# Kernel tuning notes

Hardware: AMD Instinct MI355X
Metric: run time of the kernel (lower is better)

The kernel has to match this reference:

```python
import math
import jax, jax.numpy as jnp
import numpy as np

D_MODEL = 768
N_HEADS = 12
HEAD_DIM = D_MODEL // N_HEADS
D_FF = 3072
LN_EPS = 1e-5


def _alibi_slopes(n_heads):
    def pow2(n):
        start = 2 ** (-(2 ** (-(math.log2(n) - 3))))
        return [start * start ** i for i in range(n)]
    if n_heads & (n_heads - 1) == 0:
        s = pow2(n_heads)
    else:
        c = 2 ** math.floor(math.log2(n_heads))
        s = pow2(c) + pow2(2 * c)[0::2][: n_heads - c]
    return np.asarray(s, dtype=np.float32)  # positive; negated at use site


def _ln(t, g, b):
    m = jnp.mean(t, axis=-1, keepdims=True)
    v = jnp.mean(jnp.square(t - m), axis=-1, keepdims=True)
    return (t - m) * jax.lax.rsqrt(v + LN_EPS) * g + b


def setup_inputs() -> dict:
    key = jax.random.key(0)
    ks = jax.random.split(key, 12)
    B, N = 4, 1025
    s = 0.02
    inp = {
        "x": jax.random.normal(ks[0], (B, N, D_MODEL), dtype=jnp.float32),
        "positions": jax.random.normal(ks[1], (B, N, 2), dtype=jnp.float32) * 8.0,
        "patch_sizes": jax.random.uniform(ks[2], (B,), dtype=jnp.float32, minval=0.5, maxval=2.0),
        "num_registers": 0,
        "ln1_g": jnp.ones((D_MODEL,), jnp.float32),
        "ln1_b": jnp.zeros((D_MODEL,), jnp.float32),
        "wq": jax.random.normal(ks[3], (D_MODEL, D_MODEL), jnp.float32) * s,
        "bq": jnp.zeros((D_MODEL,), jnp.float32),
        "wk": jax.random.normal(ks[4], (D_MODEL, D_MODEL), jnp.float32) * s,
        "bk": jnp.zeros((D_MODEL,), jnp.float32),
        "wv": jax.random.normal(ks[5], (D_MODEL, D_MODEL), jnp.float32) * s,
        "bv": jnp.zeros((D_MODEL,), jnp.float32),
        "wo": jax.random.normal(ks[6], (D_MODEL, D_MODEL), jnp.float32) * s,
        "bo": jnp.zeros((D_MODEL,), jnp.float32),
        "qn_g": jnp.ones((HEAD_DIM,), jnp.float32),
        "qn_b": jnp.zeros((HEAD_DIM,), jnp.float32),
        "kn_g": jnp.ones((HEAD_DIM,), jnp.float32),
        "kn_b": jnp.zeros((HEAD_DIM,), jnp.float32),
        "ln2_g": jnp.ones((D_MODEL,), jnp.float32),
        "ln2_b": jnp.zeros((D_MODEL,), jnp.float32),
        "w1": jax.random.normal(ks[7], (D_MODEL, D_FF), jnp.float32) * s,
        "b1": jnp.zeros((D_FF,), jnp.float32),
        "w2": jax.random.normal(ks[8], (D_FF, D_MODEL), jnp.float32) * s,
        "b2": jnp.zeros((D_MODEL,), jnp.float32),
    }
    return inp


def reference(x, positions, patch_sizes, num_registers,
              ln1_g, ln1_b, wq, bq, wk, bk, wv, bv, wo, bo,
              qn_g, qn_b, kn_g, kn_b, ln2_g, ln2_b, w1, b1, w2, b2):
    B, N, d = x.shape
    H, HD = N_HEADS, HEAD_DIM

    xn = _ln(x, ln1_g, ln1_b)
    q = (xn @ wq + bq).reshape(B, N, H, HD).transpose(0, 2, 1, 3)  # [B,H,N,HD]
    k = (xn @ wk + bk).reshape(B, N, H, HD).transpose(0, 2, 1, 3)
    v = (xn @ wv + bv).reshape(B, N, H, HD).transpose(0, 2, 1, 3)
    q = _ln(q, qn_g, qn_b)  # qk-norm over head_dim
    k = _ln(k, kn_g, kn_b)

    # 2-D ALiBi bias: [B,H,N,N]
    slopes = jnp.asarray(_alibi_slopes(H))  # positive
    ps = jnp.clip(patch_sizes, 1e-6)[:, None, None]
    diff = positions[:, :, None, :] - positions[:, None, :, :]  # [B,N,N,2]
    dist = jnp.sqrt(jnp.sum(jnp.square(diff), axis=-1)) / ps  # [B,N,N]
    bias = -slopes[None, :, None, None] * dist[:, None, :, :]
    idx = jnp.arange(N)
    special = (idx == 0) | ((idx >= 1) & (idx < 1 + num_registers))  # CLS + registers
    keep = (~special).astype(x.dtype)
    bias = bias * keep[None, None, :, None] * keep[None, None, None, :]

    scale = 1.0 / math.sqrt(HD)
    scores = jnp.einsum('bhqd,bhkd->bhqk', q, k) * scale + bias
    attn = jax.nn.softmax(scores, axis=-1)
    o = jnp.einsum('bhqk,bhkd->bhqd', attn, v)
    o = o.transpose(0, 2, 1, 3).reshape(B, N, d) @ wo + bo
    x = x + o

    xn2 = _ln(x, ln2_g, ln2_b)
    mlp = jax.nn.gelu(xn2 @ w1 + b1, approximate=False) @ w2 + b2
    return x + mlp
```

## Files before the change

### kernel.cpp

```cpp
#include <hip/hip_runtime.h>
#include <hip/hip_bf16.h>
#include <math.h>

typedef __attribute__((ext_vector_type(4))) float f32x4;
typedef __attribute__((ext_vector_type(8))) short short8;

#define DMODEL 768
#define NH 12
#define HD 64
#define DFF 3072
#define KVB 64
#define NSPLIT 3
#define QH 2
#define NP 1040

struct FalseC { static constexpr bool v = false; };
struct TrueC  { static constexpr bool v = true;  };

__device__ __forceinline__ short f2bf(float f) {
    union { float f; unsigned int u; } c; c.f = f;
    unsigned int r = c.u + 0x7FFFu + ((c.u >> 16) & 1u);
    return (short)(r >> 16);
}

__device__ __forceinline__ float bf2f(short s) {
    union { unsigned int u; float f; } c; c.u = ((unsigned int)(unsigned short)s) << 16;
    return c.f;
}

__device__ __forceinline__ void gload16(const void* g, void* l) {
    __builtin_amdgcn_global_load_lds((const __attribute__((address_space(1))) void*)g,
                                     (__attribute__((address_space(3))) void*)l, 16, 0, 0);
}

__device__ __forceinline__ int xcd_swz(int o, int nwg) {
    int q = nwg >> 3, r = nwg & 7, x = o & 7, i = o >> 3;
    return (x < r ? x * (q + 1) : r * (q + 1) + (x - r) * q) + i;
}

__global__ __launch_bounds__(256) void transpose_cast(const float* __restrict__ src,
                                                      short* __restrict__ dst, int K, int Nn) {
    __shared__ float tile[32][33];
    const int n0 = blockIdx.x * 32, k0 = blockIdx.y * 32;
    const int tx = threadIdx.x & 31, ty = threadIdx.x >> 5;
    #pragma unroll
    for (int i = ty; i < 32; i += 8) {
        int k = k0 + i, n = n0 + tx;
        tile[i][tx] = (k < K && n < Nn) ? src[(size_t)k * Nn + n] : 0.f;
    }
    __syncthreads();
    #pragma unroll
    for (int i = ty; i < 32; i += 8) {
        int n = n0 + i, k = k0 + tx;
        if (n < Nn && k < K) dst[(size_t)n * K + k] = f2bf(tile[tx][i]);
    }
}

__global__ void concat_bias(const float* __restrict__ bq, const float* __restrict__ bk,
                            const float* __restrict__ bv, float* __restrict__ out) {
    int i = blockIdx.x * 256 + threadIdx.x;
    if (i < 2304) out[i] = (i < 768) ? bq[i] : (i < 1536 ? bk[i - 768] : bv[i - 1536]);
}

__global__ __launch_bounds__(256) void ln_rows(const float* __restrict__ x, const float* __restrict__ g,
                                               const float* __restrict__ bb, short* __restrict__ out, int M) {
    __shared__ float red[8];
    const int row = blockIdx.x;
    const int tid = threadIdx.x;
    const float* xr = x + (size_t)row * DMODEL;
    float v[3];
    #pragma unroll
    for (int j = 0; j < 3; j++) v[j] = xr[tid + j * 256];
    float s = v[0] + v[1] + v[2];
    #pragma unroll
    for (int mk = 32; mk; mk >>= 1) s += __shfl_xor(s, mk);
    if ((tid & 63) == 0) red[tid >> 6] = s;
    __syncthreads();
    const float mean = (red[0] + red[1] + red[2] + red[3]) * (1.0f / 768.0f);
    float sq = 0.f;
    #pragma unroll
    for (int j = 0; j < 3; j++) { float d = v[j] - mean; sq += d * d; }
    #pragma unroll
    for (int mk = 32; mk; mk >>= 1) sq += __shfl_xor(sq, mk);
    if ((tid & 63) == 0) red[4 + (tid >> 6)] = sq;
    __syncthreads();
    const float var = (red[4] + red[5] + red[6] + red[7]) * (1.0f / 768.0f);
    const float rstd = rsqrtf(var + 1e-5f);
    short* orow = out + (size_t)row * DMODEL;
    #pragma unroll
    for (int j = 0; j < 3; j++) {
        int col = tid + j * 256;
        orow[col] = f2bf((v[j] - mean) * rstd * g[col] + bb[col]);
    }
}

__global__ __launch_bounds__(256) void gemm_qkv(const short* __restrict__ A, const short* __restrict__ Bt,
        const float* __restrict__ bias,
        const float* __restrict__ qg, const float* __restrict__ qb2,
        const float* __restrict__ kg, const float* __restrict__ kb2,
        short* __restrict__ Qb, short* __restrict__ Kb, short* __restrict__ Vtp,
        int M, int B, int Nseq) {
    __shared__ short As[64 * 64];
    __shared__ short Bs[128 * 64];
    const int nbx = 18, nby = (M + 63) / 64;
    const int sid = xcd_swz(blockIdx.x, nbx * nby);
    const int n0 = (sid % nbx) * 128, m0 = (sid / nbx) * 64;
    const int tid = threadIdx.x, w = tid >> 6, lane = tid & 63, g = lane >> 4, cl = lane & 15;
    const int wm = w >> 1, wn = w & 1;
    f32x4 acc[2][4];
    #pragma unroll
    for (int a = 0; a < 2; a++)
        #pragma unroll
        for (int b2 = 0; b2 < 4; b2++) acc[a][b2] = (f32x4){0.f, 0.f, 0.f, 0.f};
    for (int kk = 0; kk < 768; kk += 64) {
        #pragma unroll
        for (int c = 0; c < 1536; c += 256) {
            int ci = c + tid;
            if (ci < 512) {
                int row = ci >> 3, p = ci & 7;
                int arow = m0 + row; if (arow >= M) arow = M - 1;
                gload16(A + (size_t)arow * 768 + kk + ((p ^ (row & 7)) << 3), &As[ci * 8]);
            } else {
                int c2 = ci - 512;
                int row = c2 >> 3, p = c2 & 7;
                gload16(Bt + (size_t)(n0 + row) * 768 + kk + ((p ^ (row & 7)) << 3), &Bs[c2 * 8]);
            }
        }
        __syncthreads();
        #pragma unroll
        for (int kh = 0; kh < 2; ++kh) {
            short8 af[2], bf[4];
            #pragma unroll
            for (int mi = 0; mi < 2; mi++) {
                int ra = wm * 32 + mi * 16 + cl;
                af[mi] = *(const short8*)&As[ra * 64 + ((((kh << 2) + g) ^ (ra & 7)) << 3)];
            }
            #pragma unroll
            for (int ni = 0; ni < 4; ni++) {
                int rb = wn * 64 + ni * 16 + cl;
                bf[ni] = *(const short8*)&Bs[rb * 64 + ((((kh << 2) + g) ^ (rb & 7)) << 3)];
            }
            #pragma unroll
            for (int mi = 0; mi < 2; mi++)
                #pragma unroll
                for (int ni = 0; ni < 4; ni++)
                    acc[mi][ni] = __builtin_amdgcn_mfma_f32_16x16x32_bf16(af[mi], bf[ni], acc[mi][ni], 0, 0, 0);
        }
        __syncthreads();
    }
    const int t = n0 / 768;
    const int h = (n0 - t * 768) / 64 + wn;
    const int b0 = m0 / Nseq, bnd = (b0 + 1) * Nseq;
    float bi[4];
    #pragma unroll
    for (int ni = 0; ni < 4; ni++) bi[ni] = bias[n0 + wn * 64 + ni * 16 + cl];
    if (t < 2) {
        const float* gp = (t == 0) ? qg : kg;
        const float* bp = (t == 0) ? qb2 : kb2;
        float gv[4], bv[4];
        #pragma unroll
        for (int ni = 0; ni < 4; ni++) { gv[ni] = gp[ni * 16 + cl]; bv[ni] = bp[ni * 16 + cl]; }
        short* out = (t == 0) ? Qb : Kb;
        #pragma unroll
        for (int mi = 0; mi < 2; mi++)
            #pragma unroll
            for (int r = 0; r < 4; r++) {
                int row = m0 + wm * 32 + mi * 16 + 4 * g + r;
                float v0 = acc[mi][0][r] + bi[0];
                float v1 = acc[mi][1][r] + bi[1];
                float v2 = acc[mi][2][r] + bi[2];
                float v3 = acc[mi][3][r] + bi[3];
                float sx = v0 + v1 + v2 + v3;
                float sxx = v0 * v0 + v1 * v1 + v2 * v2 + v3 * v3;
                #pragma unroll
                for (int mk = 8; mk; mk >>= 1) { sx += __shfl_xor(sx, mk); sxx += __shfl_xor(sxx, mk); }
                float mean = sx * (1.0f / 64.0f);
                float var = sxx * (1.0f / 64.0f) - mean * mean;
                float rstd = rsqrtf(var + 1e-5f);
                if (row < M) {
                    int bb = (row >= bnd) ? b0 + 1 : b0;
                    int n = row - bb * Nseq;
                    size_t base = (((size_t)bb * NH + h) * Nseq + n) * HD + cl;
                    out[base + 0]  = f2bf(fmaf((v0 - mean) * rstd, gv[0], bv[0]));
                    out[base + 16] = f2bf(fmaf((v1 - mean) * rstd, gv[1], bv[1]));
                    out[base + 32] = f2bf(fmaf((v2 - mean) * rstd, gv[2], bv[2]));
                    out[base + 48] = f2bf(fmaf((v3 - mean) * rstd, gv[3], bv[3]));
                }
            }
    } else {
        #pragma unroll
        for (int mi = 0; mi < 2; mi++)
            #pragma unroll
            for (int r = 0; r < 4; r++) {
                int row = m0 + wm * 32 + mi * 16 + 4 * g + r;
                if (row < M) {
                    int bb = (row >= bnd) ? b0 + 1 : b0;
                    int n = row - bb * Nseq;
                    size_t vb2 = ((size_t)bb * NH + h) * HD + cl;
                    #pragma unroll
                    for (int ni = 0; ni < 4; ni++)
                        Vtp[(vb2 + ni * 16) * NP + n] = f2bf(acc[mi][ni][r] + bi[ni]);
                }
            }
    }
}

template<int EPI, int BM, int BN>
__global__ __launch_bounds__(256) void gemm_bt(const short* __restrict__ A, const short* __restrict__ Bt,
        const float* __restrict__ bias, const float* __restrict__ res, void* __restrict__ Cv,
        int M, int Nn, int K) {
    constexpr int RN = BN / 32;
    __shared__ short As[BM * 64];
    __shared__ short Bs[BN * 64];
    const int nbx = Nn / BN, nby = (M + BM - 1) / BM;
    const int sid = xcd_swz(blockIdx.x, nbx * nby);
    const int n0 = (sid % nbx) * BN, m0 = (sid / nbx) * BM;
    const int tid = threadIdx.x, w = tid >> 6, lane = tid & 63, g = lane >> 4, cl = lane & 15;
    const int wm = w >> 1, wn = w & 1;
    f32x4 acc[2][RN];
    #pragma unroll
    for (int a = 0; a < 2; a++)
        #pragma unroll
        for (int b2 = 0; b2 < RN; b2++) acc[a][b2] = (f32x4){0.f, 0.f, 0.f, 0.f};
    constexpr int CHA = BM * 8, CHT = (BM + BN) * 8;
    for (int kk = 0; kk < K; kk += 64) {
        #pragma unroll
        for (int c = 0; c < CHT; c += 256) {
            int ci = c + tid;
            if (ci < CHA) {
                int row = ci >> 3, p = ci & 7;
                int arow = m0 + row; if (arow >= M) arow = M - 1;
                gload16(A + (size_t)arow * K + kk + ((p ^ (row & 7)) << 3), &As[ci * 8]);
            } else {
                int c2 = ci - CHA;
                int row = c2 >> 3, p = c2 & 7;
                gload16(Bt + (size_t)(n0 + row) * K + kk + ((p ^ (row & 7)) << 3), &Bs[c2 * 8]);
            }
        }
        __syncthreads();
        #pragma unroll
        for (int kh = 0; kh < 2; ++kh) {
            short8 af[2], bf[RN];
            #pragma unroll
            for (int mi = 0; mi < 2; mi++) {
                int ra = wm * (BM / 2) + mi * 16 + cl;
                af[mi] = *(const short8*)&As[ra * 64 + ((((kh << 2) + g) ^ (ra & 7)) << 3)];
            }
            #pragma unroll
            for (int ni = 0; ni < RN; ni++) {
                int rb = wn * (BN / 2) + ni * 16 + cl;
                bf[ni] = *(const short8*)&Bs[rb * 64 + ((((kh << 2) + g) ^ (rb & 7)) << 3)];
            }
            #pragma unroll
            for (int mi = 0; mi < 2; mi++)
                #pragma unroll
                for (int ni = 0; ni < RN; ni++)
                    acc[mi][ni] = __builtin_amdgcn_mfma_f32_16x16x32_bf16(af[mi], bf[ni], acc[mi][ni], 0, 0, 0);
        }
        __syncthreads();
    }
    #pragma unroll
    for (int ni = 0; ni < RN; ++ni) {
        int col = n0 + wn * (BN / 2) + ni * 16 + cl;
        float bi = bias[col];
        #pragma unroll
        for (int mi = 0; mi < 2; ++mi) {
            int rb = m0 + wm * (BM / 2) + mi * 16 + 4 * g;
            #pragma unroll
            for (int r = 0; r < 4; ++r) {
                int row = rb + r;
                if (row < M) {
                    float vv = acc[mi][ni][r] + bi;
                    if (EPI == 1) {
                        vv += res[(size_t)row * Nn + col];
                        ((float*)Cv)[(size_t)row * Nn + col] = vv;
                    } else {
                        float ge = 0.5f * vv * (1.0f + erff(vv * 0.70710678118654752f));
                        ((short*)Cv)[(size_t)row * Nn + col] = f2bf(ge);
                    }
                }
            }
        }
    }
}

__global__ __launch_bounds__(256, 3) void attn_kernel(
        const short* __restrict__ Qb, const short* __restrict__ Kb, const short* __restrict__ Vt,
        const float* __restrict__ pos, const float* __restrict__ psz, const int* __restrict__ nregp,
        short* __restrict__ opart, float* __restrict__ ppart, int B, int Nn, int nwg) {
    __shared__ short Vbuf[2][QH][4096];
    __shared__ short Pl[4][QH][16][72];
    __shared__ float Rs[4][QH][16];
    const int nqt = (Nn + 63) >> 6;
    const int sid = xcd_swz(blockIdx.x, nwg);
    const int qt = sid % nqt;
    const int rem = sid / nqt;
    const int nyy = (NH / QH) * NSPLIT;
    const int yy = rem % nyy;
    const int b = rem / nyy;
    const int h0 = (yy / NSPLIT) * QH, sp = yy % NSPLIT;
    const int tid = threadIdx.x, w = tid >> 6, lane = tid & 63, g = lane >> 4, cl = lane & 15;
    const int nreg1 = 1 + nregp[0];
    const float inv_ps = 1.0f / fmaxf(psz[b], 1e-6f);
    const float sc2 = 0.125f * 1.4426950408889634f;
    const size_t bq = (size_t)b * Nn;
    const float2* __restrict__ pos2 = (const float2*)pos;
    const int q0 = qt * 64 + w * 16;

    size_t bh[QH], vb[QH];
    short8 qa[QH][2];
    float sP[QH];
    int qr = q0 + cl; if (qr > Nn - 1) qr = Nn - 1;
    const float2 qp = pos2[bq + qr];
    const float keepq = (qr < nreg1) ? 0.f : 1.f;
    #pragma unroll
    for (int hh = 0; hh < QH; hh++) {
        int h = h0 + hh;
        bh[hh] = ((size_t)b * NH + h) * (size_t)Nn;
        vb[hh] = ((size_t)b * NH + h) * (size_t)(HD * NP);
        float slope = (h < 8) ? exp2f(-(float)(h + 1)) : exp2f(-0.5f - (float)(h - 8));
        sP[hh] = slope * inv_ps * 1.4426950408889634f * keepq;
        const short* qptr = Qb + (bh[hh] + qr) * HD;
        qa[hh][0] = *(const short8*)(qptr + 8 * g);
        qa[hh][1] = *(const short8*)(qptr + 32 + 8 * g);
    }

    int qi[4];
    #pragma unroll
    for (int i = 0; i < 4; i++) qi[i] = q0 + 4 * g + i;

    f32x4 o[QH][4];
    float psum[QH] = {0.f, 0.f};
    #pragma unroll
    for (int hh = 0; hh < QH; hh++)
        #pragma unroll
        for (int c2 = 0; c2 < 4; c2++) o[hh][c2] = (f32x4){0.f, 0.f, 0.f, 0.f};

    const int ktiles = (Nn + KVB - 1) / KVB;
    const int tps = (ktiles + NSPLIT - 1) / NSPLIT;
    const int t0 = sp * tps, t1 = min(ktiles, t0 + tps);

    auto stage = [&](int buf, int kt) {
        const int kv0 = kt * KVB;
        #pragma unroll
        for (int it = 0; it < 2 * QH; ++it) {
            int idx = it * 256 + tid;
            int hh = idx >> 9, rm = idx & 511;
            int d = rm >> 3, slot = rm & 7;
            int kvs = kv0 + ((slot ^ (d & 7)) << 3);
            gload16(Vt + vb[hh] + (size_t)d * NP + kvs, &Vbuf[buf][hh][rm * 8]);
        }
    };

    stage(0, t0);
    int cur = 0;
    for (int kt = t0; kt < t1; ++kt) {
        const int kv0 = kt * KVB;
        __syncthreads();
        if (kt + 1 < t1) stage(cur ^ 1, kt + 1);

        auto qbody = [&](int qt2, auto mc, auto tc) {
            constexpr bool KMASK = decltype(mc)::v;
            constexpr bool TAIL  = decltype(tc)::v;
            const int kbase = kv0 + qt2 * 16;
            int krow = kbase + cl;
            if (TAIL) krow = min(krow, Nn - 1);
            const short* kp0 = Kb + (bh[0] + krow) * HD;
            const short* kp1 = Kb + (bh[1] + krow) * HD;
            const short8 k00 = *(const short8*)(kp0 + 8 * g);
            const short8 k01 = *(const short8*)(kp0 + 32 + 8 * g);
            const short8 k10 = *(const short8*)(kp1 + 8 * g);
            const short8 k11 = *(const short8*)(kp1 + 32 + 8 * g);
            f32x4 s0 = __builtin_amdgcn_mfma_f32_16x16x32_bf16(k00, qa[0][0], (f32x4){0.f,0.f,0.f,0.f}, 0, 0, 0);
            s0 = __builtin_amdgcn_mfma_f32_16x16x32_bf16(k01, qa[0][1], s0, 0, 0, 0);
            f32x4 s1 = __builtin_amdgcn_mfma_f32_16x16x32_bf16(k10, qa[1][0], (f32x4){0.f,0.f,0.f,0.f}, 0, 0, 0);
            s1 = __builtin_amdgcn_mfma_f32_16x16x32_bf16(k11, qa[1][1], s1, 0, 0, 0);
            const int kb4 = kbase + 4 * g;
            float p0v[4], p1v[4];
            #pragma unroll
            for (int i = 0; i < 4; i++) {
                int ki = kb4 + i;
                int kic = TAIL ? min(ki, Nn - 1) : ki;
                float2 kp2 = pos2[bq + kic];
                float dx = qp.x - kp2.x, dy = qp.y - kp2.y;
                float dist = sqrtf(fmaf(dx, dx, dy * dy));
                if (KMASK) dist *= (ki < nreg1) ? 0.f : 1.f;
                float e0 = fmaf(s0[i], sc2, -12.0f);
                e0 = fmaf(-sP[0], dist, e0);
                float p0 = exp2f(e0);
                float e1 = fmaf(s1[i], sc2, -12.0f);
                e1 = fmaf(-sP[1], dist, e1);
                float p1 = exp2f(e1);
                if (TAIL) { bool vl = ki < Nn; p0 = vl ? p0 : 0.f; p1 = vl ? p1 : 0.f; }
                psum[0] += p0; psum[1] += p1;
                p0v[i] = p0; p1v[i] = p1;
            }
            unsigned int w00, w01, w10, w11;
            asm("v_cvt_pk_bf16_f32 %0, %1, %2" : "=v"(w00) : "v"(p0v[0]), "v"(p0v[1]));
            asm("v_cvt_pk_bf16_f32 %0, %1, %2" : "=v"(w01) : "v"(p0v[2]), "v"(p0v[3]));
            asm("v_cvt_pk_bf16_f32 %0, %1, %2" : "=v"(w10) : "v"(p1v[0]), "v"(p1v[1]));
            asm("v_cvt_pk_bf16_f32 %0, %1, %2" : "=v"(w11) : "v"(p1v[2]), "v"(p1v[3]));
            *(unsigned int*)&Pl[w][0][cl][qt2 * 16 + 4 * g]     = w00;
            *(unsigned int*)&Pl[w][0][cl][qt2 * 16 + 4 * g + 2] = w01;
            *(unsigned int*)&Pl[w][1][cl][qt2 * 16 + 4 * g]     = w10;
            *(unsigned int*)&Pl[w][1][cl][qt2 * 16 + 4 * g + 2] = w11;
        };

        const bool istail = (kv0 + KVB > Nn);
        if (!istail) {
            if (kv0 < nreg1) {
                qbody(0, TrueC{}, FalseC{}); qbody(1, TrueC{}, FalseC{});
                qbody(2, TrueC{}, FalseC{}); qbody(3, TrueC{}, FalseC{});
            } else {
                qbody(0, FalseC{}, FalseC{}); qbody(1, FalseC{}, FalseC{});
                qbody(2, FalseC{}, FalseC{}); qbody(3, FalseC{}, FalseC{});
            }
        } else {
            qbody(0, FalseC{}, TrueC{}); qbody(1, FalseC{}, TrueC{});
            qbody(2, FalseC{}, TrueC{}); qbody(3, FalseC{}, TrueC{});
        }

        #pragma unroll
        for (int hh = 0; hh < QH; hh++) {
            #pragma unroll
            for (int ks = 0; ks < 2; ++ks) {
                const short8 pf = *(const short8*)&Pl[w][hh][cl][ks * 32 + 8 * g];
                #pragma unroll
                for (int c2 = 0; c2 < 4; c2++) {
                    const int d = c2 * 16 + cl;
                    const int slot = ((ks << 2) + g) ^ (cl & 7);
                    const short8 vf = *(const short8*)&Vbuf[cur][hh][d * 64 + slot * 8];
                    o[hh][c2] = __builtin_amdgcn_mfma_f32_16x16x32_bf16(pf, vf, o[hh][c2], 0, 0, 0);
                }
            }
        }
        cur ^= 1;
    }

    #pragma unroll
    for (int hh = 0; hh < QH; hh++) {
        float r = psum[hh];
        r += __shfl_xor(r, 16);
        r += __shfl_xor(r, 32);
        if (lane < 16) Rs[w][hh][lane] = r;
    }
    float4 rs0 = *(const float4*)&Rs[w][0][4 * g];
    float4 rs1 = *(const float4*)&Rs[w][1][4 * g];
    #pragma unroll
    for (int i = 0; i < 4; i++) {
        if (qi[i] < Nn) {
            #pragma unroll
            for (int hh = 0; hh < QH; hh++) {
                size_t rbase = (((size_t)sp * B + b) * NH + (h0 + hh)) * Nn + qi[i];
                #pragma unroll
                for (int c2 = 0; c2 < 4; c2++)
                    opart[rbase * HD + c2 * 16 + cl] = f2bf(o[hh][c2][i]);
                if (cl == 0) ppart[rbase] = hh ? rs1[i] : rs0[i];
            }
        }
    }
}

__global__ __launch_bounds__(256) void attn_reduce(const short* __restrict__ opart,
        const float* __restrict__ ppart, short* __restrict__ Ob, int B, int Nn) {
    const int rows = B * NH * Nn;
    const int row = blockIdx.x * 4 + (threadIdx.x >> 6);
    if (row >= rows) return;
    const int d = threadIdx.x & 63;
    const int n = row % Nn;
    const int bh = row / Nn;
    const int h = bh % NH, b = bh / NH;
    const size_t stride = (size_t)B * NH * Nn;
    float o = 0.f, p = 0.f;
    #pragma unroll
    for (int s = 0; s < NSPLIT; s++) {
        o += bf2f(opart[((size_t)s * stride + row) * HD + d]);
        p += ppart[(size_t)s * stride + row];
    }
    Ob[((size_t)b * Nn + n) * DMODEL + h * HD + d] = f2bf(o / p);
}

extern "C" void kernel_launch(void* const* d_in, const int* in_sizes, int n_in,
                              void* d_out, int out_size, void* d_ws, size_t ws_size,
                              hipStream_t stream) {
    const float* x    = (const float*)d_in[0];
    const float* pos  = (const float*)d_in[1];
    const float* psz  = (const float*)d_in[2];
    const int*   nreg = (const int*)d_in[3];
    const float* ln1g = (const float*)d_in[4];
    const float* ln1b = (const float*)d_in[5];
    const float* wq   = (const float*)d_in[6];
    const float* bq   = (const float*)d_in[7];
    const float* wk   = (const float*)d_in[8];
    const float* bk   = (const float*)d_in[9];
    const float* wv   = (const float*)d_in[10];
    const float* bv   = (const float*)d_in[11];
    const float* wo   = (const float*)d_in[12];
    const float* bo   = (const float*)d_in[13];
    const float* qng  = (const float*)d_in[14];
    const float* qnb  = (const float*)d_in[15];
    const float* kng  = (const float*)d_in[16];
    const float* knb  = (const float*)d_in[17];
    const float* ln2g = (const float*)d_in[18];
    const float* ln2b = (const float*)d_in[19];
    const float* w1   = (const float*)d_in[20];
    const float* b1   = (const float*)d_in[21];
    const float* w2   = (const float*)d_in[22];
    const float* b2   = (const float*)d_in[23];

    const int B  = in_sizes[2];
    const int Nn = in_sizes[1] / (2 * B);
    const int M  = B * Nn;

    char* ws = (char*)d_ws;
    size_t off = 0;
    auto alloc = [&](size_t bytes) -> char* {
        char* p = ws + off;
        off += (bytes + 255) & ~(size_t)255;
        return p;
    };
    short* wt_qkv   = (short*)alloc((size_t)2304 * 768 * 2);
    short* wt_o     = (short*)alloc((size_t)768 * 768 * 2);
    short* wt_1     = (short*)alloc((size_t)3072 * 768 * 2);
    short* wt_2     = (short*)alloc((size_t)768 * 3072 * 2);
    float* bias_qkv = (float*)alloc(2304 * 4);
    short* xn       = (short*)alloc((size_t)M * 768 * 2);
    short* Qb       = (short*)alloc((size_t)M * 768 * 2);
    short* Kb       = (short*)alloc((size_t)M * 768 * 2);
    short* Vt       = (short*)alloc((size_t)B * NH * HD * NP * 2 + 4096);
    short* Ob       = (short*)alloc((size_t)M * 768 * 2);
    float* x1       = (float*)alloc((size_t)M * 768 * 4);
    short* xn2      = (short*)alloc((size_t)M * 768 * 2);
    short* hmid     = (short*)alloc((size_t)M * 3072 * 2);
    float* ppart    = (float*)alloc((size_t)NSPLIT * B * NH * Nn * 4);
    short* opart    = hmid;

    dim3 blk(256);
    transpose_cast<<<dim3(24, 24), blk, 0, stream>>>(wq, wt_qkv, 768, 768);
    transpose_cast<<<dim3(24, 24), blk, 0, stream>>>(wk, wt_qkv + 768 * 768, 768, 768);
    transpose_cast<<<dim3(24, 24), blk, 0, stream>>>(wv, wt_qkv + 2 * 768 * 768, 768, 768);
    transpose_cast<<<dim3(24, 24), blk, 0, stream>>>(wo, wt_o, 768, 768);
    transpose_cast<<<dim3(96, 24), blk, 0, stream>>>(w1, wt_1, 768, 3072);
    transpose_cast<<<dim3(24, 96), blk, 0, stream>>>(w2, wt_2, 3072, 768);
    concat_bias<<<9, blk, 0, stream>>>(bq, bk, bv, bias_qkv);

    const int MB64 = (M + 63) / 64;
    ln_rows<<<M, blk, 0, stream>>>(x, ln1g, ln1b, xn, M);
    gemm_qkv<<<18 * MB64, blk, 0, stream>>>(xn, wt_qkv, bias_qkv, qng, qnb, kng, knb,
                                            Qb, Kb, Vt, M, B, Nn);
    const int nqt = (Nn + 63) / 64;
    const int anwg = nqt * (NH / QH) * NSPLIT * B;
    attn_kernel<<<anwg, blk, 0, stream>>>(Qb, Kb, Vt, pos, psz, nreg, opart, ppart, B, Nn, anwg);
    attn_reduce<<<(B * NH * Nn + 3) / 4, blk, 0, stream>>>(opart, ppart, Ob, B, Nn);
    gemm_bt<1, 64, 64><<<12 * MB64, blk, 0, stream>>>(Ob, wt_o, bo, x, x1, M, 768, 768);
    ln_rows<<<M, blk, 0, stream>>>(x1, ln2g, ln2b, xn2, M);
    gemm_bt<2, 64, 128><<<24 * MB64, blk, 0, stream>>>(xn2, wt_1, b1, nullptr, hmid, M, 3072, 768);
    gemm_bt<1, 64, 64><<<12 * MB64, blk, 0, stream>>>(hmid, wt_2, b2, x1, (float*)d_out, M, 768, 3072);
}
```

Baseline: 264.7 us.

## Shrink attention KV tile to 32, pack both heads' V in one LDS buffer

The attention kernel now processes 32 keys per tile instead of 64, with 2 KV splits instead of 3. Both heads' V slices share one 64x64 swizzled LDS buffer, and the P scratch padding is reduced. Less shared memory and fewer registers let the launch bound rise to 4 blocks per CU, aimed at better latency hiding, at the cost of more loop iterations and barriers per key. The GEMM template is also generalized to support BM other than 64 via an RM parameter.

```diff
diff --git a/kernel.cpp b/kernel.cpp
--- a/kernel.cpp
+++ b/kernel.cpp
@@ -9,8 +9,8 @@
 #define NH 12
 #define HD 64
 #define DFF 3072
-#define KVB 64
-#define NSPLIT 3
+#define KVB 32
+#define NSPLIT 2
 #define QH 2
 #define NP 1040
 
@@ -209,7 +209,7 @@
 __global__ __launch_bounds__(256) void gemm_bt(const short* __restrict__ A, const short* __restrict__ Bt,
         const float* __restrict__ bias, const float* __restrict__ res, void* __restrict__ Cv,
         int M, int Nn, int K) {
-    constexpr int RN = BN / 32;
+    constexpr int RM = BM / 32, RN = BN / 32;
     __shared__ short As[BM * 64];
     __shared__ short Bs[BN * 64];
     const int nbx = Nn / BN, nby = (M + BM - 1) / BM;
@@ -217,9 +217,9 @@
     const int n0 = (sid % nbx) * BN, m0 = (sid / nbx) * BM;
     const int tid = threadIdx.x, w = tid >> 6, lane = tid & 63, g = lane >> 4, cl = lane & 15;
     const int wm = w >> 1, wn = w & 1;
-    f32x4 acc[2][RN];
-    #pragma unroll
-    for (int a = 0; a < 2; a++)
+    f32x4 acc[RM][RN];
+    #pragma unroll
+    for (int a = 0; a < RM; a++)
         #pragma unroll
         for (int b2 = 0; b2 < RN; b2++) acc[a][b2] = (f32x4){0.f, 0.f, 0.f, 0.f};
     constexpr int CHA = BM * 8, CHT = (BM + BN) * 8;
@@ -240,9 +240,9 @@
         __syncthreads();
         #pragma unroll
         for (int kh = 0; kh < 2; ++kh) {
-            short8 af[2], bf[RN];
-            #pragma unroll
-            for (int mi = 0; mi < 2; mi++) {
+            short8 af[RM], bf[RN];
+            #pragma unroll
+            for (int mi = 0; mi < RM; mi++) {
                 int ra = wm * (BM / 2) + mi * 16 + cl;
                 af[mi] = *(const short8*)&As[ra * 64 + ((((kh << 2) + g) ^ (ra & 7)) << 3)];
             }
@@ -252,7 +252,7 @@
                 bf[ni] = *(const short8*)&Bs[rb * 64 + ((((kh << 2) + g) ^ (rb & 7)) << 3)];
             }
             #pragma unroll
-            for (int mi = 0; mi < 2; mi++)
+            for (int mi = 0; mi < RM; mi++)
                 #pragma unroll
                 for (int ni = 0; ni < RN; ni++)
                     acc[mi][ni] = __builtin_amdgcn_mfma_f32_16x16x32_bf16(af[mi], bf[ni], acc[mi][ni], 0, 0, 0);
@@ -264,7 +264,7 @@
         int col = n0 + wn * (BN / 2) + ni * 16 + cl;
         float bi = bias[col];
         #pragma unroll
-        for (int mi = 0; mi < 2; ++mi) {
+        for (int mi = 0; mi < RM; ++mi) {
             int rb = m0 + wm * (BM / 2) + mi * 16 + 4 * g;
             #pragma unroll
             for (int r = 0; r < 4; ++r) {
@@ -284,12 +284,12 @@
     }
 }
 
-__global__ __launch_bounds__(256, 3) void attn_kernel(
+__global__ __launch_bounds__(256, 4) void attn_kernel(
         const short* __restrict__ Qb, const short* __restrict__ Kb, const short* __restrict__ Vt,
         const float* __restrict__ pos, const float* __restrict__ psz, const int* __restrict__ nregp,
         short* __restrict__ opart, float* __restrict__ ppart, int B, int Nn, int nwg) {
-    __shared__ short Vbuf[2][QH][4096];
-    __shared__ short Pl[4][QH][16][72];
+    __shared__ short Vbuf[2][4096];
+    __shared__ short Pl[4][QH][16][68];
     __shared__ float Rs[4][QH][16];
     const int nqt = (Nn + 63) >> 6;
     const int sid = xcd_swz(blockIdx.x, nwg);
@@ -343,12 +343,13 @@
     auto stage = [&](int buf, int kt) {
         const int kv0 = kt * KVB;
         #pragma unroll
-        for (int it = 0; it < 2 * QH; ++it) {
+        for (int it = 0; it < 2; ++it) {
             int idx = it * 256 + tid;
-            int hh = idx >> 9, rm = idx & 511;
-            int d = rm >> 3, slot = rm & 7;
-            int kvs = kv0 + ((slot ^ (d & 7)) << 3);
-            gload16(Vt + vb[hh] + (size_t)d * NP + kvs, &Vbuf[buf][hh][rm * 8]);
+            int d = idx >> 3, s = idx & 7;
+            int u = s ^ (d & 7);
+            int hh = u >> 2;
+            int kvs = kv0 + ((u & 3) << 3);
+            gload16(Vt + vb[hh] + (size_t)d * NP + kvs, &Vbuf[buf][idx * 8]);
         }
     };
 
@@ -408,30 +409,21 @@
 
         const bool istail = (kv0 + KVB > Nn);
         if (!istail) {
-            if (kv0 < nreg1) {
-                qbody(0, TrueC{}, FalseC{}); qbody(1, TrueC{}, FalseC{});
-                qbody(2, TrueC{}, FalseC{}); qbody(3, TrueC{}, FalseC{});
-            } else {
-                qbody(0, FalseC{}, FalseC{}); qbody(1, FalseC{}, FalseC{});
-                qbody(2, FalseC{}, FalseC{}); qbody(3, FalseC{}, FalseC{});
-            }
+            if (kv0 < nreg1) { qbody(0, TrueC{}, FalseC{});  qbody(1, TrueC{}, FalseC{}); }
+            else             { qbody(0, FalseC{}, FalseC{}); qbody(1, FalseC{}, FalseC{}); }
         } else {
             qbody(0, FalseC{}, TrueC{}); qbody(1, FalseC{}, TrueC{});
-            qbody(2, FalseC{}, TrueC{}); qbody(3, FalseC{}, TrueC{});
         }
 
         #pragma unroll
         for (int hh = 0; hh < QH; hh++) {
-            #pragma unroll
-            for (int ks = 0; ks < 2; ++ks) {
-                const short8 pf = *(const short8*)&Pl[w][hh][cl][ks * 32 + 8 * g];
-                #pragma unroll
-                for (int c2 = 0; c2 < 4; c2++) {
-                    const int d = c2 * 16 + cl;
-                    const int slot = ((ks << 2) + g) ^ (cl & 7);
-                    const short8 vf = *(const short8*)&Vbuf[cur][hh][d * 64 + slot * 8];
-                    o[hh][c2] = __builtin_amdgcn_mfma_f32_16x16x32_bf16(pf, vf, o[hh][c2], 0, 0, 0);
-                }
+            const short8 pf = *(const short8*)&Pl[w][hh][cl][8 * g];
+            #pragma unroll
+            for (int c2 = 0; c2 < 4; c2++) {
+                const int d = c2 * 16 + cl;
+                const int slot = (hh * 4 + g) ^ (cl & 7);
+                const short8 vf = *(const short8*)&Vbuf[cur][d * 64 + slot * 8];
+                o[hh][c2] = __builtin_amdgcn_mfma_f32_16x16x32_bf16(pf, vf, o[hh][c2], 0, 0, 0);
             }
         }
         cur ^= 1;
```

Measured after the change: 270.5 us. 2.2% more time.

## Double-buffer shared-memory tiles in GEMMs with prefetch of next K slice

Applied to the files above, without the earlier changes.

The QKV and generic GEMM kernels now use two shared-memory buffers. Each iteration issues the next K-slice load before computing on the current one, and one of the two barriers per iteration is dropped. The QKV GEMM and the FC1 GEMM shrink the K tile to 32 to keep shared memory in check, with a 4-way XOR swizzle. The attention P scratch row padding also changes from 72 to 68. The aim is to hide global-load latency behind MFMA work, at the cost of more loop iterations and possibly different LDS bank-conflict behaviour.

```diff
diff --git a/kernel.cpp b/kernel.cpp
--- a/kernel.cpp
+++ b/kernel.cpp
@@ -100,8 +100,8 @@
         const float* __restrict__ kg, const float* __restrict__ kb2,
         short* __restrict__ Qb, short* __restrict__ Kb, short* __restrict__ Vtp,
         int M, int B, int Nseq) {
-    __shared__ short As[64 * 64];
-    __shared__ short Bs[128 * 64];
+    __shared__ short As[2][64 * 32];
+    __shared__ short Bs[2][128 * 32];
     const int nbx = 18, nby = (M + 63) / 64;
     const int sid = xcd_swz(blockIdx.x, nbx * nby);
     const int n0 = (sid % nbx) * 128, m0 = (sid / nbx) * 64;
@@ -112,42 +112,47 @@
     for (int a = 0; a < 2; a++)
         #pragma unroll
         for (int b2 = 0; b2 < 4; b2++) acc[a][b2] = (f32x4){0.f, 0.f, 0.f, 0.f};
-    for (int kk = 0; kk < 768; kk += 64) {
-        #pragma unroll
-        for (int c = 0; c < 1536; c += 256) {
+
+    auto stage = [&](int buf, int kk) {
+        #pragma unroll
+        for (int c = 0; c < 768; c += 256) {
             int ci = c + tid;
-            if (ci < 512) {
-                int row = ci >> 3, p = ci & 7;
+            if (ci < 256) {
+                int row = ci >> 2, p = ci & 3;
                 int arow = m0 + row; if (arow >= M) arow = M - 1;
-                gload16(A + (size_t)arow * 768 + kk + ((p ^ (row & 7)) << 3), &As[ci * 8]);
+                gload16(A + (size_t)arow * 768 + kk + ((p ^ (row & 3)) << 3), &As[buf][ci * 8]);
             } else {
-                int c2 = ci - 512;
-                int row = c2 >> 3, p = c2 & 7;
-                gload16(Bt + (size_t)(n0 + row) * 768 + kk + ((p ^ (row & 7)) << 3), &Bs[c2 * 8]);
-            }
-        }
+                int c2 = ci - 256;
+                int row = c2 >> 2, p = c2 & 3;
+                gload16(Bt + (size_t)(n0 + row) * 768 + kk + ((p ^ (row & 3)) << 3), &Bs[buf][c2 * 8]);
+            }
+        }
+    };
+
+    stage(0, 0);
+    int cur = 0;
+    for (int kk = 0; kk < 768; kk += 32) {
         __syncthreads();
-        #pragma unroll
-        for (int kh = 0; kh < 2; ++kh) {
-            short8 af[2], bf[4];
-            #pragma unroll
-            for (int mi = 0; mi < 2; mi++) {
-                int ra = wm * 32 + mi * 16 + cl;
-                af[mi] = *(const short8*)&As[ra * 64 + ((((kh << 2) + g) ^ (ra & 7)) << 3)];
-            }
-            #pragma unroll
-            for (int ni = 0; ni < 4; ni++) {
-                int rb = wn * 64 + ni * 16 + cl;
-                bf[ni] = *(const short8*)&Bs[rb * 64 + ((((kh << 2) + g) ^ (rb & 7)) << 3)];
-            }
-            #pragma unroll
-            for (int mi = 0; mi < 2; mi++)
-                #pragma unroll
-                for (int ni = 0; ni < 4; ni++)
-                    acc[mi][ni] = __builtin_amdgcn_mfma_f32_16x16x32_bf16(af[mi], bf[ni], acc[mi][ni], 0, 0, 0);
-        }
-        __syncthreads();
-    }
+        if (kk + 32 < 768) stage(cur ^ 1, kk + 32);
+        short8 af[2], bf[4];
+        #pragma unroll
+        for (int mi = 0; mi < 2; mi++) {
+            int ra = wm * 32 + mi * 16 + cl;
+            af[mi] = *(const short8*)&As[cur][ra * 32 + ((g ^ (ra & 3)) << 3)];
+        }
+        #pragma unroll
+        for (int ni = 0; ni < 4; ni++) {
+            int rb = wn * 64 + ni * 16 + cl;
+            bf[ni] = *(const short8*)&Bs[cur][rb * 32 + ((g ^ (rb & 3)) << 3)];
+        }
+        #pragma unroll
+        for (int mi = 0; mi < 2; mi++)
+            #pragma unroll
+            for (int ni = 0; ni < 4; ni++)
+                acc[mi][ni] = __builtin_amdgcn_mfma_f32_16x16x32_bf16(af[mi], bf[ni], acc[mi][ni], 0, 0, 0);
+        cur ^= 1;
+    }
+
     const int t = n0 / 768;
     const int h = (n0 - t * 768) / 64 + wn;
     const int b0 = m0 / Nseq, bnd = (b0 + 1) * Nseq;
@@ -205,66 +210,74 @@
     }
 }
 
-template<int EPI, int BM, int BN>
+template<int EPI, int BM, int BN, int BK>
 __global__ __launch_bounds__(256) void gemm_bt(const short* __restrict__ A, const short* __restrict__ Bt,
         const float* __restrict__ bias, const float* __restrict__ res, void* __restrict__ Cv,
         int M, int Nn, int K) {
-    constexpr int RN = BN / 32;
-    __shared__ short As[BM * 64];
-    __shared__ short Bs[BN * 64];
+    constexpr int RM = BM / 32, RN = BN / 32;
+    constexpr int SL = BK / 8, SM = SL - 1;
+    __shared__ short As[2][BM * BK];
+    __shared__ short Bs[2][BN * BK];
     const int nbx = Nn / BN, nby = (M + BM - 1) / BM;
     const int sid = xcd_swz(blockIdx.x, nbx * nby);
     const int n0 = (sid % nbx) * BN, m0 = (sid / nbx) * BM;
     const int tid = threadIdx.x, w = tid >> 6, lane = tid & 63, g = lane >> 4, cl = lane & 15;
     const int wm = w >> 1, wn = w & 1;
-    f32x4 acc[2][RN];
-    #pragma unroll
-    for (int a = 0; a < 2; a++)
+    f32x4 acc[RM][RN];
+    #pragma unroll
+    for (int a = 0; a < RM; a++)
         #pragma unroll
         for (int b2 = 0; b2 < RN; b2++) acc[a][b2] = (f32x4){0.f, 0.f, 0.f, 0.f};
-    constexpr int CHA = BM * 8, CHT = (BM + BN) * 8;
-    for (int kk = 0; kk < K; kk += 64) {
+    constexpr int CHA = BM * SL, CHT = (BM + BN) * SL;
+
+    auto stage = [&](int buf, int kk) {
         #pragma unroll
         for (int c = 0; c < CHT; c += 256) {
             int ci = c + tid;
             if (ci < CHA) {
-                int row = ci >> 3, p = ci & 7;
+                int row = ci / SL, p = ci & SM;
                 int arow = m0 + row; if (arow >= M) arow = M - 1;
-                gload16(A + (size_t)arow * K + kk + ((p ^ (row & 7)) << 3), &As[ci * 8]);
+                gload16(A + (size_t)arow * K + kk + ((p ^ (row & SM)) << 3), &As[buf][ci * 8]);
             } else {
                 int c2 = ci - CHA;
-                int row = c2 >> 3, p = c2 & 7;
-                gload16(Bt + (size_t)(n0 + row) * K + kk + ((p ^ (row & 7)) << 3), &Bs[c2 * 8]);
-            }
-        }
+                int row = c2 / SL, p = c2 & SM;
+                gload16(Bt + (size_t)(n0 + row) * K + kk + ((p ^ (row & SM)) << 3), &Bs[buf][c2 * 8]);
+            }
+        }
+    };
+
+    stage(0, 0);
+    int cur = 0;
+    for (int kk = 0; kk < K; kk += BK) {
         __syncthreads();
-        #pragma unroll
-        for (int kh = 0; kh < 2; ++kh) {
-            short8 af[2], bf[RN];
-            #pragma unroll
-            for (int mi = 0; mi < 2; mi++) {
+        if (kk + BK < K) stage(cur ^ 1, kk + BK);
+        #pragma unroll
+        for (int kh = 0; kh < BK / 32; ++kh) {
+            short8 af[RM], bf[RN];
+            #pragma unroll
+            for (int mi = 0; mi < RM; mi++) {
                 int ra = wm * (BM / 2) + mi * 16 + cl;
-                af[mi] = *(const short8*)&As[ra * 64 + ((((kh << 2) + g) ^ (ra & 7)) << 3)];
+                af[mi] = *(const short8*)&As[cur][ra * BK + ((((kh << 2) + g) ^ (ra & SM)) << 3)];
             }
             #pragma unroll
             for (int ni = 0; ni < RN; ni++) {
                 int rb = wn * (BN / 2) + ni * 16 + cl;
-                bf[ni] = *(const short8*)&Bs[rb * 64 + ((((kh << 2) + g) ^ (rb & 7)) << 3)];
-            }
-            #pragma unroll
-            for (int mi = 0; mi < 2; mi++)
+                bf[ni] = *(const short8*)&Bs[cur][rb * BK + ((((kh << 2) + g) ^ (rb & SM)) << 3)];
+            }
+            #pragma unroll
+            for (int mi = 0; mi < RM; mi++)
                 #pragma unroll
                 for (int ni = 0; ni < RN; ni++)
                     acc[mi][ni] = __builtin_amdgcn_mfma_f32_16x16x32_bf16(af[mi], bf[ni], acc[mi][ni], 0, 0, 0);
         }
-        __syncthreads();
+        cur ^= 1;
     }
     #pragma unroll
     for (int ni = 0; ni < RN; ++ni) {
         int col = n0 + wn * (BN / 2) + ni * 16 + cl;
         float bi = bias[col];
         #pragma unroll
-        for (int mi = 0; mi < 2; ++mi) {
+        for (int mi = 0; mi < RM; ++mi) {
             int rb = m0 + wm * (BM / 2) + mi * 16 + 4 * g;
             #pragma unroll
             for (int r = 0; r < 4; ++r) {
@@ -289,7 +302,7 @@
         const float* __restrict__ pos, const float* __restrict__ psz, const int* __restrict__ nregp,
         short* __restrict__ opart, float* __restrict__ ppart, int B, int Nn, int nwg) {
     __shared__ short Vbuf[2][QH][4096];
-    __shared__ short Pl[4][QH][16][72];
+    __shared__ short Pl[4][QH][16][68];
     __shared__ float Rs[4][QH][16];
     const int nqt = (Nn + 63) >> 6;
     const int sid = xcd_swz(blockIdx.x, nwg);
@@ -552,8 +565,8 @@
     const int anwg = nqt * (NH / QH) * NSPLIT * B;
     attn_kernel<<<anwg, blk, 0, stream>>>(Qb, Kb, Vt, pos, psz, nreg, opart, ppart, B, Nn, anwg);
     attn_reduce<<<(B * NH * Nn + 3) / 4, blk, 0, stream>>>(opart, ppart, Ob, B, Nn);
-    gemm_bt<1, 64, 64><<<12 * MB64, blk, 0, stream>>>(Ob, wt_o, bo, x, x1, M, 768, 768);
+    gemm_bt<1, 64, 64, 64><<<12 * MB64, blk, 0, stream>>>(Ob, wt_o, bo, x, x1, M, 768, 768);
     ln_rows<<<M, blk, 0, stream>>>(x1, ln2g, ln2b, xn2, M);
-    gemm_bt<2, 64, 128><<<24 * MB64, blk, 0, stream>>>(xn2, wt_1, b1, nullptr, hmid, M, 3072, 768);
-    gemm_bt<1, 64, 64><<<12 * MB64, blk, 0, stream>>>(hmid, wt_2, b2, x1, (float*)d_out, M, 768, 3072);
-}
+    gemm_bt<2, 64, 128, 32><<<24 * MB64, blk, 0, stream>>>(xn2, wt_1, b1, nullptr, hmid, M, 3072, 768);
+    gemm_bt<1, 64, 64, 64><<<12 * MB64, blk, 0, stream>>>(hmid, wt_2, b2, x1, (float*)d_out, M, 768, 3072);
+}
```

Result: slower. 284.3 us (+7.4%).
